# Performance work log

Measured on AMD Instinct MI355X. Metric: run time of the kernel, lower is better.

Reference implementation:

```python
import jax, jax.numpy as jnp
import numpy as np

CHANNELS = 512
NUM_HEADS = 8
GROUPS = 32
EPS = 1e-5


def setup_inputs() -> dict:
    key = jax.random.key(0)
    ks = jax.random.split(key, 7)
    C = CHANNELS
    x = jax.random.normal(ks[0], (8, C, 32, 32), dtype=jnp.float32)
    gn_weight = jnp.ones((C,), dtype=jnp.float32)
    gn_bias = jnp.zeros((C,), dtype=jnp.float32)
    # Conv1d(C, 3C, k=1) weights ~ N(0, 0.02) per init_weights
    qkv_w = 0.02 * jax.random.normal(ks[1], (3 * C, C), dtype=jnp.float32)
    qkv_b = 0.01 * jax.random.normal(ks[2], (3 * C,), dtype=jnp.float32)
    out_w = 0.02 * jax.random.normal(ks[3], (C, C), dtype=jnp.float32)
    out_b = 0.01 * jax.random.normal(ks[4], (C,), dtype=jnp.float32)
    return {"x": x, "gn_weight": gn_weight, "gn_bias": gn_bias,
            "qkv_w": qkv_w, "qkv_b": qkv_b, "out_w": out_w, "out_b": out_b}


def _forward(x, gn_weight, gn_bias, qkv_w, qkv_b, out_w, out_b):
    n, c, h, w = x.shape
    hw = h * w
    heads = NUM_HEADS
    cph = c // heads
    xs = x.reshape(n, c, hw)  # [N, C, HW]
    # GroupNorm over (channels-in-group, spatial)
    xg = xs.reshape(n, GROUPS, c // GROUPS, hw)
    mean = jnp.mean(xg, axis=(2, 3), keepdims=True)
    var = jnp.var(xg, axis=(2, 3), keepdims=True)
    xn = ((xg - mean) * jax.lax.rsqrt(var + EPS)).reshape(n, c, hw)
    xn = xn * gn_weight[None, :, None] + gn_bias[None, :, None]
    # 1x1 Conv1d QKV projection
    qkv = jnp.einsum('oc,ncl->nol', qkv_w, xn) + qkv_b[None, :, None]  # [N, 3C, HW]
    q, k, v = jnp.split(qkv, 3, axis=1)  # each [N, C, HW]
    q = q.reshape(n * heads, cph, hw)
    k = k.reshape(n * heads, cph, hw)
    v = v.reshape(n * heads, cph, hw)
    scale = 1.0 / np.sqrt(cph).astype(np.float32)
    scores = jnp.einsum('bci,bcj->bij', q, k) * scale  # [NH, HW, HW]
    attn = jax.nn.softmax(scores, axis=-1)
    weighted = jnp.einsum('bij,bcj->bic', attn, v)  # [NH, HW, cph]
    # Faithful to torch: reshape(n, -1, h, w) on [n*heads, hw, cph] layout
    weighted = weighted.reshape(n, c, h, w)
    out = jnp.einsum('oc,nchw->nohw', out_w, weighted) + out_b[None, :, None, None]
    return out


def reference(x, gn_weight, gn_bias, qkv_w, qkv_b, out_w, out_b):
    return _forward(x, gn_weight, gn_bias, qkv_w, qkv_b, out_w, out_b)
```

## Files before the change

### kernel.cpp

```cpp
#include <hip/hip_runtime.h>
#include <math.h>

#define N_    8
#define C_    512
#define HW_   1024
#define G_    32
#define CPG_  16
#define OC3_  1536
#define LOG2E 1.44269504f

typedef _Float16 f16;
typedef f16 f16x8 __attribute__((ext_vector_type(8)));
typedef f16 f16x4 __attribute__((ext_vector_type(4)));
typedef float f32x4 __attribute__((ext_vector_type(4)));

#define GLOAD_LDS16(g, l)                                                          \
    __builtin_amdgcn_global_load_lds(                                              \
        (const __attribute__((address_space(1))) unsigned int*)(const void*)(g),   \
        (__attribute__((address_space(3))) unsigned int*)(void*)(l), 16, 0, 0)

#define WAIT_VM0() __builtin_amdgcn_s_waitcnt(0x0F70)

__global__ __launch_bounds__(256) void prep(const float* __restrict__ x,
                                            const float* __restrict__ gw,
                                            const float* __restrict__ gb,
                                            f16* __restrict__ XT,
                                            const float* __restrict__ qkv_w,
                                            const float* __restrict__ out_w,
                                            const float* __restrict__ qkv_b,
                                            f16* __restrict__ Wq,
                                            f16* __restrict__ Wo,
                                            float* __restrict__ qkv_bs) {
    __shared__ float red1[4], red2[4];
    __shared__ float sm, srstd;
    if (blockIdx.x >= 256) {
        const float QS = 0.125f * LOG2E;
        int idx = (blockIdx.x - 256) * 256 + threadIdx.x;
        if (idx < 786432) {
            float v = qkv_w[idx];
            if (idx < 262144) v *= QS;
            Wq[idx] = (f16)v;
        } else if (idx < 786432 + 262144) {
            Wo[idx - 786432] = (f16)out_w[idx - 786432];
        } else if (idx < 786432 + 262144 + 1536) {
            int i = idx - 786432 - 262144;
            float v = qkv_b[i];
            if (i < 512) v *= QS;
            qkv_bs[i] = v;
        }
        return;
    }
    int blk = blockIdx.x;
    int n = blk >> 5, g = blk & 31;
    size_t base = ((size_t)n * C_ + (size_t)g * CPG_) * HW_;
    const float4* xp4 = (const float4*)(x + base);
    float4 vals[16];
    float s1 = 0.f, s2 = 0.f;
#pragma unroll
    for (int r = 0; r < 16; r++) {
        float4 v = xp4[r * 256 + threadIdx.x];
        vals[r] = v;
        s1 += v.x + v.y + v.z + v.w;
        s2 += v.x * v.x + v.y * v.y + v.z * v.z + v.w * v.w;
    }
#pragma unroll
    for (int off = 32; off > 0; off >>= 1) {
        s1 += __shfl_down(s1, off, 64);
        s2 += __shfl_down(s2, off, 64);
    }
    int wave = threadIdx.x >> 6, lane = threadIdx.x & 63;
    if (lane == 0) { red1[wave] = s1; red2[wave] = s2; }
    __syncthreads();
    if (threadIdx.x == 0) {
        float t1 = red1[0] + red1[1] + red1[2] + red1[3];
        float t2 = red2[0] + red2[1] + red2[2] + red2[3];
        float mean = t1 * (1.f / 16384.f);
        float var  = t2 * (1.f / 16384.f) - mean * mean;
        sm = mean;
        srstd = rsqrtf(var + 1e-5f);
    }
    __syncthreads();
    float mean = sm, rstd = srstd;
    float av[16], bbv[16];
#pragma unroll
    for (int r = 0; r < 16; r++) {
        int c = g * CPG_ + r;
        av[r] = gw[c] * rstd;
        bbv[r] = gb[c] - mean * av[r];
    }
    f16x8 lo[4], hi[4];
#pragma unroll
    for (int r = 0; r < 16; r++) {
        float4 v = vals[r];
        float a = av[r], bb = bbv[r];
        f16 e0 = (f16)(v.x * a + bb), e1 = (f16)(v.y * a + bb);
        f16 e2 = (f16)(v.z * a + bb), e3 = (f16)(v.w * a + bb);
        if (r < 8) { lo[0][r] = e0; lo[1][r] = e1; lo[2][r] = e2; lo[3][r] = e3; }
        else { hi[0][r - 8] = e0; hi[1][r - 8] = e1; hi[2][r - 8] = e2; hi[3][r - 8] = e3; }
    }
    f16* xt = XT + ((size_t)n * HW_ + (size_t)threadIdx.x * 4) * C_ + g * CPG_;
#pragma unroll
    for (int comp = 0; comp < 4; comp++) {
        *(f16x8*)&xt[(size_t)comp * C_]     = lo[comp];
        *(f16x8*)&xt[(size_t)comp * C_ + 8] = hi[comp];
    }
}

template <bool FINAL>
__global__ __launch_bounds__(256, 4) void gemm_f16(const f16* __restrict__ A,
                                                   const f16* __restrict__ B,
                                                   const float* __restrict__ bias,
                                                   void* __restrict__ Yq,
                                                   f16* __restrict__ Yv) {
    __shared__ __align__(16) unsigned char smem[34816];
    f16* As = (f16*)smem;
    f16* Bs = (f16*)(smem + 16384);
    int tid = threadIdx.x, lane = tid & 63, w = tid >> 6;
    int m = lane & 15, quad = lane >> 4;
    int ow0 = (w & 1) * 64, lw0 = (w >> 1) * 64;
    int flat = blockIdx.x;
    int n = flat & 7, rest = flat >> 3;
    int l0 = (rest & 7) * 128, o0 = (rest >> 3) * 128;
    const f16* Bn = B + ((size_t)n * HW_ + l0) * 512;

    int rowT[4], sgT[4];
#pragma unroll
    for (int t = 0; t < 4; t++) {
        int q = (w * 4 + t) * 64 + lane;
        int row = q >> 3, seg = q & 7;
        rowT[t] = row;
        sgT[t] = seg ^ (row & 7);
    }

    f32x4 acc[4][4];
#pragma unroll
    for (int i = 0; i < 4; i++)
#pragma unroll
        for (int j = 0; j < 4; j++)
#pragma unroll
            for (int r = 0; r < 4; r++) acc[i][j][r] = 0.f;

    for (int c0 = 0; c0 < 512; c0 += 64) {
        __syncthreads();
#pragma unroll
        for (int t = 0; t < 4; t++) {
            GLOAD_LDS16(A + (size_t)(o0 + rowT[t]) * 512 + c0 + sgT[t] * 8,
                        As + (size_t)(w * 4 + t) * 512);
            GLOAD_LDS16(Bn + (size_t)rowT[t] * 512 + c0 + sgT[t] * 8,
                        Bs + (size_t)(w * 4 + t) * 512);
        }
        WAIT_VM0();
        __syncthreads();
#pragma unroll
        for (int ks = 0; ks < 2; ks++) {
            f16x8 af[4], bf[4];
#pragma unroll
            for (int ib = 0; ib < 4; ib++) {
                int row = ow0 + ib * 16 + m;
                int seg = (ks * 4 + quad) ^ (row & 7);
                af[ib] = *(const f16x8*)&As[row * 64 + seg * 8];
            }
#pragma unroll
            for (int jb = 0; jb < 4; jb++) {
                int row = lw0 + jb * 16 + m;
                int seg = (ks * 4 + quad) ^ (row & 7);
                bf[jb] = *(const f16x8*)&Bs[row * 64 + seg * 8];
            }
#pragma unroll
            for (int ib = 0; ib < 4; ib++)
#pragma unroll
                for (int jb = 0; jb < 4; jb++)
                    acc[ib][jb] = __builtin_amdgcn_mfma_f32_16x16x32_f16(
                        af[ib], bf[jb], acc[ib][jb], 0, 0, 0);
        }
    }

    float bv[4][4];
#pragma unroll
    for (int ib = 0; ib < 4; ib++)
#pragma unroll
        for (int r = 0; r < 4; r++)
            bv[ib][r] = bias[o0 + ow0 + ib * 16 + quad * 4 + r];

    if (FINAL) {
        float* on = (float*)Yq + (size_t)n * C_ * HW_;
#pragma unroll
        for (int ib = 0; ib < 4; ib++)
#pragma unroll
            for (int jb = 0; jb < 4; jb++)
#pragma unroll
                for (int r = 0; r < 4; r++)
                    on[(size_t)(o0 + ow0 + ib * 16 + quad * 4 + r) * HW_ +
                       l0 + lw0 + jb * 16 + m] = acc[ib][jb][r] + bv[ib][r];
    } else if (o0 >= 1024) {
        f16* vn = Yv + (size_t)n * C_ * HW_;
#pragma unroll
        for (int ib = 0; ib < 4; ib++)
#pragma unroll
            for (int jb = 0; jb < 4; jb++)
#pragma unroll
                for (int r = 0; r < 4; r++)
                    vn[(size_t)(o0 - 1024 + ow0 + ib * 16 + quad * 4 + r) * HW_ +
                       l0 + lw0 + jb * 16 + m] = (f16)(acc[ib][jb][r] + bv[ib][r]);
    } else {
        __syncthreads();
        f16* T = (f16*)smem;
#pragma unroll
        for (int ib = 0; ib < 4; ib++)
#pragma unroll
            for (int jb = 0; jb < 4; jb++) {
                f16x4 h;
#pragma unroll
                for (int r = 0; r < 4; r++) h[r] = (f16)(acc[ib][jb][r] + bv[ib][r]);
                int l = lw0 + jb * 16 + m;
                int oo = ow0 + ib * 16 + quad * 4;
                *(f16x4*)&T[l * 136 + oo] = h;
            }
        __syncthreads();
        f16* qn = (f16*)Yq + (size_t)n * HW_ * 1024;
#pragma unroll
        for (int rep = 0; rep < 8; rep++) {
            int idx = rep * 256 + tid;
            int l = idx >> 4, seg = idx & 15;
            f16x8 v = *(const f16x8*)&T[l * 136 + seg * 8];
            *(f16x8*)&qn[(size_t)(l0 + l) * 1024 + o0 + seg * 8] = v;
        }
    }
}

__global__ __launch_bounds__(256, 4) void attn_f16(const f16* __restrict__ qkvT,
                                                   const f16* __restrict__ vbuf,
                                                   f16* __restrict__ w2T) {
    __shared__ __align__(16) unsigned char smem[40960];
    f16* Kb0  = (f16*)smem;
    f16* Vb0  = (f16*)(smem + 16384);
    f16* Ps   = (f16*)(smem + 32768);
    f16* LDSo = (f16*)smem;

    int tid = threadIdx.x;
    int lane = tid & 63, wave = tid >> 6;
    int m = lane & 15, quad = lane >> 4;
    int iw = wave * 16;
    int flat = blockIdx.x;
    int xcd = flat & 7, slot = flat >> 3;
    int itile = slot >> 3, bh = (slot & 7) * 8 + xcd;
    int n = bh >> 3, head = bh & 7;
    int i0 = itile * 64;
    const f16* qb = qkvT + (size_t)n * HW_ * 1024 + head * 64;
    const f16* kb = qb + 512;
    const f16* vb = vbuf + (size_t)n * C_ * HW_ + (size_t)head * 64 * HW_;
    f16* PsW = Ps + iw * 64;

    f16x8 aq0 = *(const f16x8*)&qb[(size_t)(i0 + iw + m) * 1024 + quad * 8];
    f16x8 aq1 = *(const f16x8*)&qb[(size_t)(i0 + iw + m) * 1024 + 32 + quad * 8];

#pragma unroll
    for (int it = 0; it < 2; it++) {
        int chunk = it * 256 + tid;
        int row = chunk >> 3, seg = chunk & 7;
        int segg = seg ^ (row & 7);
        GLOAD_LDS16(kb + (size_t)row * 1024 + segg * 8,
                    Kb0 + ((size_t)it * 256 + wave * 64) * 8);
        GLOAD_LDS16(vb + (size_t)row * HW_ + segg * 8,
                    Vb0 + ((size_t)it * 256 + wave * 64) * 8);
    }

    f32x4 oacc[4];
#pragma unroll
    for (int cb = 0; cb < 4; cb++)
#pragma unroll
        for (int r = 0; r < 4; r++) oacc[cb][r] = 0.f;
    float lsum = 0.f;

    for (int jt = 0; jt < 16; jt++) {
        int p = jt & 1;
        const f16* Kp = Kb0 + p * 4096;
        const f16* Vp = Vb0 + p * 4096;
        WAIT_VM0();
        __syncthreads();
        if (jt < 15) {
            int j0n = (jt + 1) * 64;
            f16* Kn = Kb0 + (1 - p) * 4096;
            f16* Vn = Vb0 + (1 - p) * 4096;
#pragma unroll
            for (int it = 0; it < 2; it++) {
                int chunk = it * 256 + tid;
                int row = chunk >> 3, seg = chunk & 7;
                int segg = seg ^ (row & 7);
                GLOAD_LDS16(kb + (size_t)(j0n + row) * 1024 + segg * 8,
                            Kn + ((size_t)it * 256 + wave * 64) * 8);
                GLOAD_LDS16(vb + (size_t)row * HW_ + j0n + segg * 8,
                            Vn + ((size_t)it * 256 + wave * 64) * 8);
            }
        }

        f32x4 sacc[4];
#pragma unroll
        for (int jb = 0; jb < 4; jb++)
#pragma unroll
            for (int r = 0; r < 4; r++) sacc[jb][r] = 0.f;
#pragma unroll
        for (int jb = 0; jb < 4; jb++) {
            int row = jb * 16 + m;
            f16x8 k0 = *(const f16x8*)&Kp[row * 64 + ((quad ^ (row & 7)) * 8)];
            sacc[jb] = __builtin_amdgcn_mfma_f32_16x16x32_f16(k0, aq0, sacc[jb], 0, 0, 0);
        }
#pragma unroll
        for (int jb = 0; jb < 4; jb++) {
            int row = jb * 16 + m;
            f16x8 k1 = *(const f16x8*)&Kp[row * 64 + (((4 + quad) ^ (row & 7)) * 8)];
            sacc[jb] = __builtin_amdgcn_mfma_f32_16x16x32_f16(k1, aq1, sacc[jb], 0, 0, 0);
        }

#pragma unroll
        for (int jb = 0; jb < 4; jb++) {
            f16x4 h;
#pragma unroll
            for (int r = 0; r < 4; r++) {
                float pv = exp2f(sacc[jb][r]);
                h[r] = (f16)pv;
                lsum += pv;
            }
            int seg = jb * 4 + quad;
            *(f16x4*)&PsW[m * 64 + ((seg ^ (m & 7)) * 4)] = h;
        }

#pragma unroll
        for (int ks = 0; ks < 2; ks++) {
            int s0 = ks * 8 + quad * 2;
            f16x4 apl = *(const f16x4*)&PsW[m * 64 + ((s0 ^ (m & 7)) * 4)];
            f16x4 aph = *(const f16x4*)&PsW[m * 64 + (((s0 + 1) ^ (m & 7)) * 4)];
            f16x8 ap = {apl[0], apl[1], apl[2], apl[3], aph[0], aph[1], aph[2], aph[3]};
#pragma unroll
            for (int cb = 0; cb < 4; cb++) {
                int vrow = cb * 16 + m;
                f16x8 bvv = *(const f16x8*)&Vp[vrow * 64 +
                                               (((ks * 4 + quad) ^ (vrow & 7)) * 8)];
                oacc[cb] = __builtin_amdgcn_mfma_f32_16x16x32_f16(ap, bvv, oacc[cb], 0, 0, 0);
            }
        }
    }

    float ls = lsum;
    ls += __shfl_xor(ls, 16, 64);
    ls += __shfl_xor(ls, 32, 64);
    float linv[4];
#pragma unroll
    for (int r = 0; r < 4; r++)
        linv[r] = 1.f / __shfl(ls, quad * 4 + r, 64);
    WAIT_VM0();
    __syncthreads();
#pragma unroll
    for (int cb = 0; cb < 4; cb++)
#pragma unroll
        for (int r = 0; r < 4; r++) {
            int s = (quad * 4 + r) * 64 + cb * 16 + m;
            LDSo[s * 4 + wave] = (f16)(oacc[cb][r] * linv[r]);
        }
    __syncthreads();
    f16* w2n = w2T + (size_t)n * HW_ * 512;
    int chbase = head * 64 + (i0 >> 4);
#pragma unroll
    for (int it = 0; it < 4; it++) {
        int s = it * 256 + tid;
        *(f16x4*)&w2n[(size_t)s * 512 + chbase] = *(const f16x4*)&LDSo[s * 4];
    }
}

extern "C" void kernel_launch(void* const* d_in, const int* in_sizes, int n_in,
                              void* d_out, int out_size, void* d_ws, size_t ws_size,
                              hipStream_t stream) {
    (void)in_sizes; (void)n_in; (void)out_size; (void)ws_size;
    const float* x     = (const float*)d_in[0];
    const float* gw    = (const float*)d_in[1];
    const float* gb    = (const float*)d_in[2];
    const float* qkv_w = (const float*)d_in[3];
    const float* qkv_b = (const float*)d_in[4];
    const float* out_w = (const float*)d_in[5];
    const float* out_b = (const float*)d_in[6];
    float* out = (float*)d_out;
    char* ws = (char*)d_ws;

    const size_t MB = 1024 * 1024;
    f16*   qkvT   = (f16*)ws;
    f16*   XT     = (f16*)(ws + 16 * MB);
    f16*   vbuf   = (f16*)(ws + 24 * MB);
    f16*   w2T    = (f16*)(ws + 32 * MB);
    f16*   Wq     = (f16*)(ws + 40 * MB);
    f16*   Wo     = (f16*)(ws + 42 * MB);
    float* qkv_bs = (float*)(ws + 43 * MB);

    prep<<<dim3(256 + 4103), 256, 0, stream>>>(x, gw, gb, XT,
                                               qkv_w, out_w, qkv_b, Wq, Wo, qkv_bs);
    gemm_f16<false><<<dim3(768), 256, 0, stream>>>(Wq, XT, qkv_bs, (void*)qkvT, vbuf);
    attn_f16<<<dim3(1024), 256, 0, stream>>>(qkvT, vbuf, w2T);
    gemm_f16<true><<<dim3(256), 256, 0, stream>>>(Wo, w2T, out_b, (void*)out, nullptr);
}
```

Measured before the change: 155.6 us.

## Double query rows per attention block to reuse K/V tiles across two sub-tiles

Each attention block now handles 128 query rows instead of 64. Each wave processes two 16-row sub-tiles and reuses the K fragments it loaded into registers for both. The grid is halved to 512 blocks, which halves the global K/V traffic and LDS staging per output row. The cost is more registers per wave (two sets of output accumulators), larger shared memory (48KB), fewer blocks for latency hiding, and a wider f16x8 output store.

```diff
diff --git a/kernel.cpp b/kernel.cpp
--- a/kernel.cpp
+++ b/kernel.cpp
@@ -231,7 +231,7 @@
 __global__ __launch_bounds__(256, 4) void attn_f16(const f16* __restrict__ qkvT,
                                                    const f16* __restrict__ vbuf,
                                                    f16* __restrict__ w2T) {
-    __shared__ __align__(16) unsigned char smem[40960];
+    __shared__ __align__(16) unsigned char smem[49152];
     f16* Kb0  = (f16*)smem;
     f16* Vb0  = (f16*)(smem + 16384);
     f16* Ps   = (f16*)(smem + 32768);
@@ -240,19 +240,22 @@
     int tid = threadIdx.x;
     int lane = tid & 63, wave = tid >> 6;
     int m = lane & 15, quad = lane >> 4;
-    int iw = wave * 16;
     int flat = blockIdx.x;
     int xcd = flat & 7, slot = flat >> 3;
     int itile = slot >> 3, bh = (slot & 7) * 8 + xcd;
     int n = bh >> 3, head = bh & 7;
-    int i0 = itile * 64;
+    int i0 = itile * 128;
     const f16* qb = qkvT + (size_t)n * HW_ * 1024 + head * 64;
     const f16* kb = qb + 512;
     const f16* vb = vbuf + (size_t)n * C_ * HW_ + (size_t)head * 64 * HW_;
-    f16* PsW = Ps + iw * 64;
-
-    f16x8 aq0 = *(const f16x8*)&qb[(size_t)(i0 + iw + m) * 1024 + quad * 8];
-    f16x8 aq1 = *(const f16x8*)&qb[(size_t)(i0 + iw + m) * 1024 + 32 + quad * 8];
+
+    f16x8 aq[2][2];
+#pragma unroll
+    for (int s = 0; s < 2; s++) {
+        const f16* qr = qb + (size_t)(i0 + wave * 32 + s * 16 + m) * 1024;
+        aq[s][0] = *(const f16x8*)&qr[quad * 8];
+        aq[s][1] = *(const f16x8*)&qr[32 + quad * 8];
+    }
 
 #pragma unroll
     for (int it = 0; it < 2; it++) {
@@ -265,12 +268,14 @@
                     Vb0 + ((size_t)it * 256 + wave * 64) * 8);
     }
 
-    f32x4 oacc[4];
-#pragma unroll
-    for (int cb = 0; cb < 4; cb++)
-#pragma unroll
-        for (int r = 0; r < 4; r++) oacc[cb][r] = 0.f;
-    float lsum = 0.f;
+    f32x4 oacc[2][4];
+#pragma unroll
+    for (int s = 0; s < 2; s++)
+#pragma unroll
+        for (int cb = 0; cb < 4; cb++)
+#pragma unroll
+            for (int r = 0; r < 4; r++) oacc[s][cb][r] = 0.f;
+    float lsum[2] = {0.f, 0.f};
 
     for (int jt = 0; jt < 16; jt++) {
         int p = jt & 1;
@@ -294,76 +299,91 @@
             }
         }
 
-        f32x4 sacc[4];
-#pragma unroll
-        for (int jb = 0; jb < 4; jb++)
-#pragma unroll
-            for (int r = 0; r < 4; r++) sacc[jb][r] = 0.f;
+        f16x8 kf[8];
 #pragma unroll
         for (int jb = 0; jb < 4; jb++) {
             int row = jb * 16 + m;
-            f16x8 k0 = *(const f16x8*)&Kp[row * 64 + ((quad ^ (row & 7)) * 8)];
-            sacc[jb] = __builtin_amdgcn_mfma_f32_16x16x32_f16(k0, aq0, sacc[jb], 0, 0, 0);
-        }
-#pragma unroll
-        for (int jb = 0; jb < 4; jb++) {
-            int row = jb * 16 + m;
-            f16x8 k1 = *(const f16x8*)&Kp[row * 64 + (((4 + quad) ^ (row & 7)) * 8)];
-            sacc[jb] = __builtin_amdgcn_mfma_f32_16x16x32_f16(k1, aq1, sacc[jb], 0, 0, 0);
-        }
-
-#pragma unroll
-        for (int jb = 0; jb < 4; jb++) {
-            f16x4 h;
-#pragma unroll
-            for (int r = 0; r < 4; r++) {
-                float pv = exp2f(sacc[jb][r]);
-                h[r] = (f16)pv;
-                lsum += pv;
-            }
-            int seg = jb * 4 + quad;
-            *(f16x4*)&PsW[m * 64 + ((seg ^ (m & 7)) * 4)] = h;
-        }
-
-#pragma unroll
-        for (int ks = 0; ks < 2; ks++) {
-            int s0 = ks * 8 + quad * 2;
-            f16x4 apl = *(const f16x4*)&PsW[m * 64 + ((s0 ^ (m & 7)) * 4)];
-            f16x4 aph = *(const f16x4*)&PsW[m * 64 + (((s0 + 1) ^ (m & 7)) * 4)];
-            f16x8 ap = {apl[0], apl[1], apl[2], apl[3], aph[0], aph[1], aph[2], aph[3]};
-#pragma unroll
-            for (int cb = 0; cb < 4; cb++) {
-                int vrow = cb * 16 + m;
-                f16x8 bvv = *(const f16x8*)&Vp[vrow * 64 +
-                                               (((ks * 4 + quad) ^ (vrow & 7)) * 8)];
-                oacc[cb] = __builtin_amdgcn_mfma_f32_16x16x32_f16(ap, bvv, oacc[cb], 0, 0, 0);
-            }
-        }
-    }
-
-    float ls = lsum;
-    ls += __shfl_xor(ls, 16, 64);
-    ls += __shfl_xor(ls, 32, 64);
-    float linv[4];
-#pragma unroll
-    for (int r = 0; r < 4; r++)
-        linv[r] = 1.f / __shfl(ls, quad * 4 + r, 64);
+            kf[jb]     = *(const f16x8*)&Kp[row * 64 + ((quad ^ (row & 7)) * 8)];
+            kf[4 + jb] = *(const f16x8*)&Kp[row * 64 + (((4 + quad) ^ (row & 7)) * 8)];
+        }
+
+#pragma unroll
+        for (int s = 0; s < 2; s++) {
+            f16* PsW = Ps + (size_t)(wave * 2 + s) * 1024;
+            f32x4 sacc[4];
+#pragma unroll
+            for (int jb = 0; jb < 4; jb++)
+#pragma unroll
+                for (int r = 0; r < 4; r++) sacc[jb][r] = 0.f;
+#pragma unroll
+            for (int jb = 0; jb < 4; jb++)
+                sacc[jb] = __builtin_amdgcn_mfma_f32_16x16x32_f16(kf[jb], aq[s][0],
+                                                                  sacc[jb], 0, 0, 0);
+#pragma unroll
+            for (int jb = 0; jb < 4; jb++)
+                sacc[jb] = __builtin_amdgcn_mfma_f32_16x16x32_f16(kf[4 + jb], aq[s][1],
+                                                                  sacc[jb], 0, 0, 0);
+
+#pragma unroll
+            for (int jb = 0; jb < 4; jb++) {
+                f16x4 h;
+#pragma unroll
+                for (int r = 0; r < 4; r++) {
+                    float pv = exp2f(sacc[jb][r]);
+                    h[r] = (f16)pv;
+                    lsum[s] += pv;
+                }
+                int seg = jb * 4 + quad;
+                *(f16x4*)&PsW[m * 64 + ((seg ^ (m & 7)) * 4)] = h;
+            }
+
+#pragma unroll
+            for (int ks = 0; ks < 2; ks++) {
+                int s0 = ks * 8 + quad * 2;
+                f16x4 apl = *(const f16x4*)&PsW[m * 64 + ((s0 ^ (m & 7)) * 4)];
+                f16x4 aph = *(const f16x4*)&PsW[m * 64 + (((s0 + 1) ^ (m & 7)) * 4)];
+                f16x8 ap = {apl[0], apl[1], apl[2], apl[3],
+                            aph[0], aph[1], aph[2], aph[3]};
+#pragma unroll
+                for (int cb = 0; cb < 4; cb++) {
+                    int vrow = cb * 16 + m;
+                    f16x8 bvv = *(const f16x8*)&Vp[vrow * 64 +
+                                                   (((ks * 4 + quad) ^ (vrow & 7)) * 8)];
+                    oacc[s][cb] = __builtin_amdgcn_mfma_f32_16x16x32_f16(
+                        ap, bvv, oacc[s][cb], 0, 0, 0);
+                }
+            }
+        }
+    }
+
+    float linv[2][4];
+#pragma unroll
+    for (int s = 0; s < 2; s++) {
+        float ls = lsum[s];
+        ls += __shfl_xor(ls, 16, 64);
+        ls += __shfl_xor(ls, 32, 64);
+#pragma unroll
+        for (int r = 0; r < 4; r++)
+            linv[s][r] = 1.f / __shfl(ls, quad * 4 + r, 64);
+    }
     WAIT_VM0();
     __syncthreads();
 #pragma unroll
-    for (int cb = 0; cb < 4; cb++)
-#pragma unroll
-        for (int r = 0; r < 4; r++) {
-            int s = (quad * 4 + r) * 64 + cb * 16 + m;
-            LDSo[s * 4 + wave] = (f16)(oacc[cb][r] * linv[r]);
-        }
+    for (int s = 0; s < 2; s++)
+#pragma unroll
+        for (int cb = 0; cb < 4; cb++)
+#pragma unroll
+            for (int r = 0; r < 4; r++) {
+                int sc = (quad * 4 + r) * 64 + cb * 16 + m;
+                LDSo[sc * 8 + wave * 2 + s] = (f16)(oacc[s][cb][r] * linv[s][r]);
+            }
     __syncthreads();
     f16* w2n = w2T + (size_t)n * HW_ * 512;
     int chbase = head * 64 + (i0 >> 4);
 #pragma unroll
     for (int it = 0; it < 4; it++) {
-        int s = it * 256 + tid;
-        *(f16x4*)&w2n[(size_t)s * 512 + chbase] = *(const f16x4*)&LDSo[s * 4];
+        int sc = it * 256 + tid;
+        *(f16x8*)&w2n[(size_t)sc * 512 + chbase] = *(const f16x8*)&LDSo[sc * 8];
     }
 }
 
@@ -393,6 +413,6 @@
     prep<<<dim3(256 + 4103), 256, 0, stream>>>(x, gw, gb, XT,
                                                qkv_w, out_w, qkv_b, Wq, Wo, qkv_bs);
     gemm_f16<false><<<dim3(768), 256, 0, stream>>>(Wq, XT, qkv_bs, (void*)qkvT, vbuf);
-    attn_f16<<<dim3(1024), 256, 0, stream>>>(qkvT, vbuf, w2T);
+    attn_f16<<<dim3(512), 256, 0, stream>>>(qkvT, vbuf, w2T);
     gemm_f16<true><<<dim3(256), 256, 0, stream>>>(Wo, w2T, out_b, (void*)out, nullptr);
 }
```

New measurement: 155.7 us. No clear change (+0.1%).
